# Optimization experiments

Hardware: AMD Instinct MI355X
Metric: run time of the kernel (lower is better)

The kernel has to match this reference:

```python
import jax, jax.numpy as jnp
import numpy as np

N = 50000      # nodes
E = 800000     # edges (before self loops)
F_IN = 128     # num_features
D = 128        # d_graph_layer
L = 3          # n_graph_layer (extra GAT layers after conv1)
DFC = 128      # d_FC_layer
NFC = 2        # n_FC_layer
C = 2          # num_classes
G = 1000       # number of graphs
NEG_SLOPE = 0.2


def setup_inputs() -> dict:
    key = jax.random.key(0)
    ks = jax.random.split(key, 24)
    s = lambda d: 1.0 / np.sqrt(d)
    inp = {
        "x": jax.random.normal(ks[0], (N, F_IN), jnp.float32),
        "energy": jax.random.normal(ks[1], (G, 1), jnp.float32),
        # conv1 params
        "W1": jax.random.normal(ks[2], (F_IN, D), jnp.float32) * s(F_IN),
        "as1": jax.random.normal(ks[3], (D,), jnp.float32) * s(D),
        "ad1": jax.random.normal(ks[4], (D,), jnp.float32) * s(D),
        "b1": jnp.zeros((D,), jnp.float32),
        # stacked convs params
        "Ws": jax.random.normal(ks[5], (L, D, D), jnp.float32) * s(D),
        "ass": jax.random.normal(ks[6], (L, D), jnp.float32) * s(D),
        "ads": jax.random.normal(ks[7], (L, D), jnp.float32) * s(D),
        "bs": jnp.zeros((L, D), jnp.float32),
        # FC head
        "lin0_W": jax.random.normal(ks[8], (D, DFC), jnp.float32) * s(D),
        "lin0_b": jnp.zeros((DFC,), jnp.float32),
        "lin1_W": jax.random.normal(ks[9], (DFC + 1, DFC), jnp.float32) * s(DFC + 1),
        "lin1_b": jnp.zeros((DFC,), jnp.float32),
        "lins_W": jax.random.normal(ks[10], (NFC - 1, DFC, DFC), jnp.float32) * s(DFC),
        "lins_b": jnp.zeros((NFC - 1, DFC), jnp.float32),
        "lin3_W": jax.random.normal(ks[11], (DFC, C), jnp.float32) * s(DFC),
        "lin3_b": jnp.zeros((C,), jnp.float32),
        # graph structure
        "edge_index": jax.random.randint(ks[12], (2, E), 0, N, dtype=jnp.int64),
        "batchs": jnp.sort(jax.random.randint(ks[13], (N,), 0, G, dtype=jnp.int64)),
    }
    return inp


def gat_layer(x, W, a_src, a_dst, b, src, dst):
    # GATConv (heads=1): h = xW; e_ij = LeakyReLU(a_src.h_src + a_dst.h_dst);
    # alpha = softmax over edges grouped by dst; out_i = sum alpha * h_src + b
    h = x @ W                                        # [N, D]
    e = jax.nn.leaky_relu((h @ a_src)[src] + (h @ a_dst)[dst], NEG_SLOPE)  # [E']
    m = jax.ops.segment_max(e, dst, num_segments=N)  # every node has a self loop
    w = jnp.exp(e - m[dst])
    denom = jax.ops.segment_sum(w, dst, num_segments=N)
    alpha = w / denom[dst]
    out = jax.ops.segment_sum(h[src] * alpha[:, None], dst, num_segments=N)
    return out + b


def reference(x, energy, W1, as1, ad1, b1, Ws, ass, ads, bs,
              lin0_W, lin0_b, lin1_W, lin1_b, lins_W, lins_b,
              lin3_W, lin3_b, edge_index, batchs):
    loop = jnp.arange(N, dtype=edge_index.dtype)     # GATConv add_self_loops
    src = jnp.concatenate([edge_index[0], loop])
    dst = jnp.concatenate([edge_index[1], loop])

    h = jax.nn.relu(gat_layer(x, W1, as1, ad1, b1, src, dst))
    for i in range(L):
        h = jax.nn.relu(gat_layer(h, Ws[i], ass[i], ads[i], bs[i], src, dst))

    g = jax.ops.segment_sum(h, batchs, num_segments=G)   # global_add_pool [G, D]
    y = jax.nn.relu(g @ lin0_W + lin0_b)                 # lins[0]
    z = jax.nn.relu(jnp.concatenate([y, energy], axis=1) @ lin1_W + lin1_b)
    z = z + y                                            # residual
    for i in range(NFC - 1):
        z = jax.nn.relu(z @ lins_W[i] + lins_b[i])
    logits = z @ lin3_W + lin3_b
    return jax.nn.log_softmax(logits, axis=1)            # last == 'log'
```

## Files before the change

kernel.cpp:

```cpp
#include <hip/hip_runtime.h>
#include <math.h>

#define NN 50000
#define EE 800000
#define ET 850000
#define DD 128
#define GG 1000
#define SLOPE 0.2f

#define KB   2048
#define NBA  416
#define BSZ  4096
#define NBUK 208

#define LSTR 136

typedef unsigned int  u32;
typedef unsigned short u16;
typedef _Float16 f16;
typedef __attribute__((ext_vector_type(8))) _Float16 f16x8;
typedef __attribute__((ext_vector_type(4))) float f32x4;

__device__ __forceinline__ u16 f2h(float f){
  return __builtin_bit_cast(unsigned short, (_Float16)f);
}
__device__ __forceinline__ float hlo(u32 d){
  return (float)__builtin_bit_cast(_Float16, (unsigned short)(d & 0xFFFFu));
}
__device__ __forceinline__ float hhi(u32 d){
  return (float)__builtin_bit_cast(_Float16, (unsigned short)(d >> 16));
}

__global__ void init_k(const int* __restrict__ batchs, int* __restrict__ cnt,
                       int* __restrict__ gstart, int* __restrict__ bcur){
  int n = blockIdx.x*256 + threadIdx.x;
  if (n < NBUK) bcur[n] = 0;
  if (n < NN){
    cnt[n] = 0;
    int b = batchs[n];
    int prev = n ? batchs[n-1] : -1;
    for (int g = prev+1; g <= b; ++g) gstart[g] = n;
    if (n == NN-1){
      for (int g = b+1; g <= GG; ++g) gstart[g] = NN;
    }
  }
}

__global__ void count_k(const int* __restrict__ ei, int* __restrict__ cnt,
                        int* __restrict__ rank){
  int e = blockIdx.x*256 + threadIdx.x;
  if (e < ET){
    int d = (e < EE) ? ei[EE + e] : (e - EE);
    rank[e] = atomicAdd(&cnt[d], 1);
  }
}

__global__ __launch_bounds__(256) void blocksum_k(const int* __restrict__ cnt,
                                                  int* __restrict__ bsum){
  int i = blockIdx.x*256 + threadIdx.x;
  int v = (i < NN) ? cnt[i] : 0;
  #pragma unroll
  for (int o=32;o;o>>=1) v += __shfl_xor(v,o);
  __shared__ int ws[4];
  if ((threadIdx.x & 63) == 0) ws[threadIdx.x>>6] = v;
  __syncthreads();
  if (threadIdx.x == 0) bsum[blockIdx.x] = ws[0]+ws[1]+ws[2]+ws[3];
}

__global__ __launch_bounds__(256) void scanb_k(int* __restrict__ bsum, int nb){
  int tid = threadIdx.x;
  int v = (tid < nb) ? bsum[tid] : 0;
  int lane = tid & 63, wv = tid >> 6;
  int s = v;
  #pragma unroll
  for (int o=1;o<64;o<<=1){ int t = __shfl_up(s,o); if (lane>=o) s += t; }
  __shared__ int ws[4];
  if (lane == 63) ws[wv] = s;
  __syncthreads();
  int woff = 0;
  for (int k=0;k<wv;++k) woff += ws[k];
  if (tid < nb) bsum[tid] = s - v + woff;
}

__global__ __launch_bounds__(256) void scatter_k(const int* __restrict__ cnt,
                                                 const int* __restrict__ bsum,
                                                 int* __restrict__ row_start){
  int i = blockIdx.x*256 + threadIdx.x;
  int v = (i < NN) ? cnt[i] : 0;
  int lane = threadIdx.x & 63, wv = threadIdx.x >> 6;
  int s = v;
  #pragma unroll
  for (int o=1;o<64;o<<=1){ int t = __shfl_up(s,o); if (lane>=o) s += t; }
  __shared__ int ws[4];
  if (lane == 63) ws[wv] = s;
  __syncthreads();
  int woff = 0;
  for (int k=0;k<wv;++k) woff += ws[k];
  int off = s - v + woff + bsum[blockIdx.x];
  if (i < NN) row_start[i] = off;
  if (i == 0) row_start[NN] = ET;
}

__global__ __launch_bounds__(256) void partA_k(const int* __restrict__ ei,
                                               const int* __restrict__ rank,
                                               const int* __restrict__ row_start,
                                               int* __restrict__ bcur,
                                               uint2* __restrict__ stage){
  __shared__ uint2 lpairs[KB];
  __shared__ int lcnt[256], lstart[256], lrun[256], gbase[256];
  __shared__ int ws[4];
  int tid = threadIdx.x;
  int base = blockIdx.x * KB;
  int nE = min(KB, ET - base);
  lcnt[tid] = 0;
  __syncthreads();
  u32 pos_r[KB/256]; u32 src_r[KB/256];
  #pragma unroll
  for (int i=0;i<KB/256;++i){
    int e = base + i*256 + tid;
    u32 p = 0xFFFFFFFFu, s = 0;
    if (e < ET){
      int d, sr;
      if (e < EE){ sr = ei[e]; d = ei[EE + e]; }
      else       { sr = e - EE; d = sr; }
      p = (u32)(row_start[d] + rank[e]);
      s = (u32)sr;
      atomicAdd(&lcnt[p >> 12], 1);
    }
    pos_r[i] = p; src_r[i] = s;
  }
  __syncthreads();
  int v = lcnt[tid];
  int lane = tid & 63, wv = tid >> 6;
  int s = v;
  #pragma unroll
  for (int o=1;o<64;o<<=1){ int t = __shfl_up(s,o); if (lane>=o) s += t; }
  if (lane == 63) ws[wv] = s;
  __syncthreads();
  int woff = 0;
  for (int k=0;k<wv;++k) woff += ws[k];
  int excl = s - v + woff;
  lstart[tid] = excl;
  lrun[tid]   = excl;
  gbase[tid]  = (tid < NBUK && v > 0) ? atomicAdd(&bcur[tid], v) : 0;
  __syncthreads();
  #pragma unroll
  for (int i=0;i<KB/256;++i){
    if (pos_r[i] != 0xFFFFFFFFu){
      int b = pos_r[i] >> 12;
      int slot = atomicAdd(&lrun[b], 1);
      lpairs[slot] = make_uint2(pos_r[i], src_r[i]);
    }
  }
  __syncthreads();
  for (int j = tid; j < nE; j += 256){
    uint2 pr = lpairs[j];
    int b = pr.x >> 12;
    int dest = (b << 12) + gbase[b] + (j - lstart[b]);
    stage[dest] = pr;
  }
}

__global__ __launch_bounds__(256) void partB_k(const uint2* __restrict__ stage,
                                               int* __restrict__ srcs){
  __shared__ int buf[BSZ];
  int b = blockIdx.x, tid = threadIdx.x;
  int base = b << 12;
  int n_b = min(BSZ, ET - base);
  for (int j = tid; j < n_b; j += 256){
    uint2 pr = stage[base + j];
    buf[pr.x - base] = (int)pr.y;
  }
  __syncthreads();
  for (int j = tid; j*4 < n_b; j += 256){
    *(int4*)(srcs + base + j*4) = *(const int4*)(buf + j*4);
  }
}

__global__ __launch_bounds__(256) void gemm_mfma_k(const float* __restrict__ A,
                                                   const float* __restrict__ W,
                                                   const float* __restrict__ as,
                                                   const float* __restrict__ ad,
                                                   u16* __restrict__ Ch,
                                                   float* __restrict__ hs,
                                                   float* __restrict__ hd){
  __shared__ u16 Al[64*LSTR];
  __shared__ u16 Wt[128*LSTR];
  int tid = threadIdx.x;
  int rbase = blockIdx.x*64;

  #pragma unroll
  for (int it=0; it<8; ++it){
    int i = it*256 + tid;
    int r = i >> 5, c4 = i & 31;
    float4 v = {0.f,0.f,0.f,0.f};
    if (rbase + r < NN) v = *(const float4*)(A + (size_t)(rbase+r)*DD + c4*4);
    u32 p0 = (u32)f2h(v.x) | ((u32)f2h(v.y) << 16);
    u32 p1 = (u32)f2h(v.z) | ((u32)f2h(v.w) << 16);
    *(u32*)(&Al[r*LSTR + c4*4])     = p0;
    *(u32*)(&Al[r*LSTR + c4*4 + 2]) = p1;
  }
  #pragma unroll
  for (int it=0; it<16; ++it){
    int i = it*256 + tid;
    int k = i >> 5, c4 = i & 31;
    float4 v = *(const float4*)(W + (size_t)k*DD + c4*4);
    Wt[(c4*4+0)*LSTR + k] = f2h(v.x);
    Wt[(c4*4+1)*LSTR + k] = f2h(v.y);
    Wt[(c4*4+2)*LSTR + k] = f2h(v.z);
    Wt[(c4*4+3)*LSTR + k] = f2h(v.w);
  }
  __syncthreads();

  int wid = tid >> 6;
  int l   = tid & 63;
  int lr  = l & 15;
  int lk  = l >> 4;

  f32x4 acc[8] = {};
  #pragma unroll
  for (int ks=0; ks<4; ++ks){
    int k0 = ks*32;
    f16x8 a = *(const f16x8*)(&Al[(wid*16+lr)*LSTR + k0 + lk*8]);
    #pragma unroll
    for (int ct=0; ct<8; ++ct){
      f16x8 b = *(const f16x8*)(&Wt[(ct*16+lr)*LSTR + k0 + lk*8]);
      acc[ct] = __builtin_amdgcn_mfma_f32_16x16x32_f16(a, b, acc[ct], 0, 0, 0);
    }
  }

  float hsum[4] = {0.f,0.f,0.f,0.f};
  float hdsum[4] = {0.f,0.f,0.f,0.f};
  #pragma unroll
  for (int ct=0; ct<8; ++ct){
    float a_s = as[ct*16 + lr];
    float a_d = ad[ct*16 + lr];
    #pragma unroll
    for (int i=0;i<4;++i){
      hsum[i]  += acc[ct][i]*a_s;
      hdsum[i] += acc[ct][i]*a_d;
    }
  }
  #pragma unroll
  for (int i=0;i<4;++i){
    #pragma unroll
    for (int o=1;o<16;o<<=1){
      hsum[i]  += __shfl_xor(hsum[i],  o);
      hdsum[i] += __shfl_xor(hdsum[i], o);
    }
  }
  if (lr == 0){
    #pragma unroll
    for (int i=0;i<4;++i){
      int r = rbase + wid*16 + lk*4 + i;
      if (r < NN){ hs[r] = hsum[i]; hd[r] = hdsum[i]; }
    }
  }
  #pragma unroll
  for (int i=0;i<4;++i){
    int r = rbase + wid*16 + lk*4 + i;
    if (r < NN){
      #pragma unroll
      for (int ct=0; ct<8; ++ct)
        Ch[(size_t)r*DD + ct*16 + lr] = f2h(acc[ct][i]);
    }
  }
}

__global__ __launch_bounds__(256) void gat_agg_h_k(const u16* __restrict__ hh,
                                                   const float* __restrict__ hs,
                                                   const float* __restrict__ hd,
                                                   const int* __restrict__ row_start,
                                                   const int* __restrict__ srcs,
                                                   const float* __restrict__ bias,
                                                   float* __restrict__ out){
  int node = blockIdx.x*4 + (threadIdx.x >> 6);
  int lane = threadIdx.x & 63;
  if (node >= NN) return;
  int half = lane >> 5;
  int hl   = lane & 31;
  int beg = row_start[node], end = row_start[node+1];
  float hdn = hd[node];
  float m = -INFINITY, denom = 0.f;
  float a0=0.f, a1=0.f, a2=0.f, a3=0.f;
  for (int c=beg; c<end; c+=64){
    int nc = min(64, end-c);
    float e = -INFINITY; int src = 0;
    if (lane < nc){
      src = srcs[c+lane];
      float t = hs[src] + hdn;
      e = (t >= 0.f) ? t : SLOPE*t;
    }
    float cm = e;
    #pragma unroll
    for (int o=32;o;o>>=1) cm = fmaxf(cm, __shfl_xor(cm,o));
    float nm = fmaxf(m, cm);
    float w = (lane < nc) ? expf(e - nm) : 0.f;
    float cs = w;
    #pragma unroll
    for (int o=32;o;o>>=1) cs += __shfl_xor(cs,o);
    float scale = expf(m - nm);
    denom = denom*scale + cs;
    a0 *= scale; a1 *= scale; a2 *= scale; a3 *= scale;
    m = nm;
    int nh = (nc + 1 - half) >> 1;
    for (int i=0;i<nh;++i){
      int j = 2*i + half;
      float wi = __shfl(w, j);
      int   si = __shfl(src, j);
      uint2 hv = *(const uint2*)(hh + (size_t)si*DD + hl*4);
      a0 += wi*hlo(hv.x); a1 += wi*hhi(hv.x);
      a2 += wi*hlo(hv.y); a3 += wi*hhi(hv.y);
    }
  }
  a0 += __shfl_xor(a0, 32);
  a1 += __shfl_xor(a1, 32);
  a2 += __shfl_xor(a2, 32);
  a3 += __shfl_xor(a3, 32);
  if (half == 0){
    float inv = 1.f/denom;
    float4 b4 = *(const float4*)(bias + hl*4);
    float4 o4;
    o4.x = fmaxf(a0*inv + b4.x, 0.f);
    o4.y = fmaxf(a1*inv + b4.y, 0.f);
    o4.z = fmaxf(a2*inv + b4.z, 0.f);
    o4.w = fmaxf(a3*inv + b4.w, 0.f);
    *(float4*)(out + (size_t)node*DD + hl*4) = o4;
  }
}

__global__ __launch_bounds__(128) void tail_k(const float* __restrict__ h,
                                              const int* __restrict__ gstart,
                                              const float* __restrict__ energy,
                                              const float* __restrict__ W0, const float* __restrict__ b0,
                                              const float* __restrict__ W1, const float* __restrict__ b1,
                                              const float* __restrict__ W2, const float* __restrict__ b2,
                                              const float* __restrict__ W3, const float* __restrict__ b3,
                                              float* __restrict__ out){
  __shared__ float row[DD];
  __shared__ float buf[DD];
  int gr = blockIdx.x, j = threadIdx.x;
  int beg = gstart[gr], end = gstart[gr+1];
  float s = 0.f;
  for (int n=beg; n<end; ++n) s += h[(size_t)n*DD + j];
  row[j] = s;
  __syncthreads();
  float acc = 0.f;
  #pragma unroll 8
  for (int k=0;k<DD;++k) acc += row[k]*W0[k*DD + j];
  float y = fmaxf(acc + b0[j], 0.f);
  buf[j] = y;
  __syncthreads();
  acc = 0.f;
  #pragma unroll 8
  for (int k=0;k<DD;++k) acc += buf[k]*W1[k*DD + j];
  acc += energy[gr]*W1[DD*DD + j];
  float z = fmaxf(acc + b1[j], 0.f) + y;
  __syncthreads();
  row[j] = z;
  __syncthreads();
  acc = 0.f;
  #pragma unroll 8
  for (int k=0;k<DD;++k) acc += row[k]*W2[k*DD + j];
  float z2 = fmaxf(acc + b2[j], 0.f);
  buf[j] = z2;
  __syncthreads();
  if (j < 64){
    float za = buf[j], zb = buf[j+64];
    float l0 = za*W3[j*2]     + zb*W3[(j+64)*2];
    float l1 = za*W3[j*2 + 1] + zb*W3[(j+64)*2 + 1];
    #pragma unroll
    for (int o=32;o;o>>=1){ l0 += __shfl_xor(l0,o); l1 += __shfl_xor(l1,o); }
    if (j == 0){
      l0 += b3[0]; l1 += b3[1];
      float mx = fmaxf(l0, l1);
      float lse = mx + logf(expf(l0-mx) + expf(l1-mx));
      out[gr*2]   = l0 - lse;
      out[gr*2+1] = l1 - lse;
    }
  }
}

extern "C" void kernel_launch(void* const* d_in, const int* in_sizes, int n_in,
                              void* d_out, int out_size, void* d_ws, size_t ws_size,
                              hipStream_t stream) {
  const float* x      = (const float*)d_in[0];
  const float* energy = (const float*)d_in[1];
  const float* W1     = (const float*)d_in[2];
  const float* as1    = (const float*)d_in[3];
  const float* ad1    = (const float*)d_in[4];
  const float* b1     = (const float*)d_in[5];
  const float* Ws     = (const float*)d_in[6];
  const float* ass    = (const float*)d_in[7];
  const float* ads    = (const float*)d_in[8];
  const float* bs     = (const float*)d_in[9];
  const float* lin0_W = (const float*)d_in[10];
  const float* lin0_b = (const float*)d_in[11];
  const float* lin1_W = (const float*)d_in[12];
  const float* lin1_b = (const float*)d_in[13];
  const float* lins_W = (const float*)d_in[14];
  const float* lins_b = (const float*)d_in[15];
  const float* lin3_W = (const float*)d_in[16];
  const float* lin3_b = (const float*)d_in[17];
  const int*   ei     = (const int*)d_in[18];
  const int*   batchs = (const int*)d_in[19];
  float* out = (float*)d_out;

  char* wp = (char*)d_ws;
  auto alloc = [&](size_t bytes)->void*{
    void* p = (void*)wp;
    wp += (bytes + 255) & ~(size_t)255;
    return p;
  };
  float* hA        = (float*)alloc((size_t)NN*DD*4);
  float* hB        = (float*)alloc((size_t)NN*DD*4);
  u16*   hHf       = (u16*)hB;
  float* hs        = (float*)alloc((size_t)NN*4);
  float* hd        = (float*)alloc((size_t)NN*4);
  int*   cnt       = (int*)alloc((size_t)NN*4);
  int*   row_start = (int*)alloc((size_t)(NN+1)*4);
  int*   rank      = (int*)alloc((size_t)ET*4);
  int*   srcs      = (int*)alloc((size_t)ET*4);
  uint2* stage     = (uint2*)alloc((size_t)NBUK*BSZ*8);
  int*   bcur      = (int*)alloc((size_t)NBUK*4);
  int*   gstart    = (int*)alloc((size_t)(GG+1)*4);
  int*   bsum      = (int*)alloc((size_t)256*4);

  const int NB_N  = (NN + 255)/256;
  const int NB_E  = (ET + 255)/256;
  const int NB_W  = (NN + 3)/4;
  const int NB_G  = (NN + 63)/64;

  init_k<<<NB_N, 256, 0, stream>>>(batchs, cnt, gstart, bcur);
  count_k<<<NB_E, 256, 0, stream>>>(ei, cnt, rank);
  blocksum_k<<<NB_N, 256, 0, stream>>>(cnt, bsum);
  scanb_k<<<1, 256, 0, stream>>>(bsum, NB_N);
  scatter_k<<<NB_N, 256, 0, stream>>>(cnt, bsum, row_start);
  partA_k<<<NBA, 256, 0, stream>>>(ei, rank, row_start, bcur, stage);
  partB_k<<<NBUK, 256, 0, stream>>>(stage, srcs);

  gemm_mfma_k<<<NB_G, 256, 0, stream>>>(x, W1, as1, ad1, hHf, hs, hd);
  gat_agg_h_k<<<NB_W, 256, 0, stream>>>(hHf, hs, hd, row_start, srcs, b1, hA);
  for (int l=1; l<4; ++l){
    const float* Wl  = Ws  + (size_t)(l-1)*DD*DD;
    const float* asl = ass + (size_t)(l-1)*DD;
    const float* adl = ads + (size_t)(l-1)*DD;
    const float* bl  = bs  + (size_t)(l-1)*DD;
    gemm_mfma_k<<<NB_G, 256, 0, stream>>>(hA, Wl, asl, adl, hHf, hs, hd);
    gat_agg_h_k<<<NB_W, 256, 0, stream>>>(hHf, hs, hd, row_start, srcs, bl, hA);
  }

  tail_k<<<GG, 128, 0, stream>>>(hA, gstart, energy,
                                 lin0_W, lin0_b, lin1_W, lin1_b,
                                 lins_W, lins_b, lin3_W, lin3_b, out);
}
```

Measured before the change: 481.8 us.

## Store activations in fp16 and pre-transpose weights; GEMM reads operands directly

```diff
diff --git a/kernel.cpp b/kernel.cpp
--- a/kernel.cpp
+++ b/kernel.cpp
@@ -13,8 +13,6 @@
 #define BSZ  4096
 #define NBUK 208
 
-#define LSTR 136
-
 typedef unsigned int  u32;
 typedef unsigned short u16;
 typedef _Float16 f16;
@@ -29,6 +27,9 @@
 }
 __device__ __forceinline__ float hhi(u32 d){
   return (float)__builtin_bit_cast(_Float16, (unsigned short)(d >> 16));
+}
+__device__ __forceinline__ float h2f(u16 h){
+  return (float)__builtin_bit_cast(_Float16, h);
 }
 
 __global__ void init_k(const int* __restrict__ batchs, int* __restrict__ cnt,
@@ -177,55 +178,58 @@
   }
 }
 
-__global__ __launch_bounds__(256) void gemm_mfma_k(const float* __restrict__ A,
-                                                   const float* __restrict__ W,
-                                                   const float* __restrict__ as,
-                                                   const float* __restrict__ ad,
-                                                   u16* __restrict__ Ch,
-                                                   float* __restrict__ hs,
-                                                   float* __restrict__ hd){
-  __shared__ u16 Al[64*LSTR];
-  __shared__ u16 Wt[128*LSTR];
+__global__ __launch_bounds__(256) void wcvt_k(const float* __restrict__ W1,
+                                              const float* __restrict__ Ws,
+                                              u16* __restrict__ Wt4){
+  int g = blockIdx.x*256 + threadIdx.x;
+  int l = g >> 14;
+  int rem = g & 16383;
+  int n = rem >> 7, k = rem & 127;
+  float v = (l == 0) ? W1[k*DD + n] : Ws[(size_t)(l-1)*DD*DD + k*DD + n];
+  Wt4[(size_t)l*DD*DD + n*DD + k] = f2h(v);
+}
+
+__global__ __launch_bounds__(256) void xcvt_k(const float* __restrict__ x,
+                                              u16* __restrict__ xh){
+  int i = blockIdx.x*256 + threadIdx.x;
+  if (i*4 < NN*DD){
+    float4 v = *(const float4*)(x + (size_t)i*4);
+    u32 p0 = (u32)f2h(v.x) | ((u32)f2h(v.y) << 16);
+    u32 p1 = (u32)f2h(v.z) | ((u32)f2h(v.w) << 16);
+    *(u32*)(xh + (size_t)i*4)     = p0;
+    *(u32*)(xh + (size_t)i*4 + 2) = p1;
+  }
+}
+
+__global__ __launch_bounds__(256) void gemm_direct_k(const u16* __restrict__ Ah,
+                                                     const u16* __restrict__ Wt,
+                                                     const float* __restrict__ as,
+                                                     const float* __restrict__ ad,
+                                                     u16* __restrict__ Ch,
+                                                     float* __restrict__ hs,
+                                                     float* __restrict__ hd){
   int tid = threadIdx.x;
   int rbase = blockIdx.x*64;
-
-  #pragma unroll
-  for (int it=0; it<8; ++it){
-    int i = it*256 + tid;
-    int r = i >> 5, c4 = i & 31;
-    float4 v = {0.f,0.f,0.f,0.f};
-    if (rbase + r < NN) v = *(const float4*)(A + (size_t)(rbase+r)*DD + c4*4);
-    u32 p0 = (u32)f2h(v.x) | ((u32)f2h(v.y) << 16);
-    u32 p1 = (u32)f2h(v.z) | ((u32)f2h(v.w) << 16);
-    *(u32*)(&Al[r*LSTR + c4*4])     = p0;
-    *(u32*)(&Al[r*LSTR + c4*4 + 2]) = p1;
-  }
-  #pragma unroll
-  for (int it=0; it<16; ++it){
-    int i = it*256 + tid;
-    int k = i >> 5, c4 = i & 31;
-    float4 v = *(const float4*)(W + (size_t)k*DD + c4*4);
-    Wt[(c4*4+0)*LSTR + k] = f2h(v.x);
-    Wt[(c4*4+1)*LSTR + k] = f2h(v.y);
-    Wt[(c4*4+2)*LSTR + k] = f2h(v.z);
-    Wt[(c4*4+3)*LSTR + k] = f2h(v.w);
-  }
-  __syncthreads();
-
   int wid = tid >> 6;
   int l   = tid & 63;
   int lr  = l & 15;
   int lk  = l >> 4;
+  int arow = rbase + wid*16 + lr;
+
+  f16x8 a[4] = {};
+  if (arow < NN){
+    #pragma unroll
+    for (int ks=0; ks<4; ++ks)
+      a[ks] = *(const f16x8*)(Ah + (size_t)arow*DD + ks*32 + lk*8);
+  }
 
   f32x4 acc[8] = {};
   #pragma unroll
-  for (int ks=0; ks<4; ++ks){
-    int k0 = ks*32;
-    f16x8 a = *(const f16x8*)(&Al[(wid*16+lr)*LSTR + k0 + lk*8]);
-    #pragma unroll
-    for (int ct=0; ct<8; ++ct){
-      f16x8 b = *(const f16x8*)(&Wt[(ct*16+lr)*LSTR + k0 + lk*8]);
-      acc[ct] = __builtin_amdgcn_mfma_f32_16x16x32_f16(a, b, acc[ct], 0, 0, 0);
+  for (int ct=0; ct<8; ++ct){
+    #pragma unroll
+    for (int ks=0; ks<4; ++ks){
+      f16x8 b = *(const f16x8*)(Wt + (size_t)(ct*16+lr)*DD + ks*32 + lk*8);
+      acc[ct] = __builtin_amdgcn_mfma_f32_16x16x32_f16(a[ks], b, acc[ct], 0, 0, 0);
     }
   }
 
@@ -273,7 +277,7 @@
                                                    const int* __restrict__ row_start,
                                                    const int* __restrict__ srcs,
                                                    const float* __restrict__ bias,
-                                                   float* __restrict__ out){
+                                                   u16* __restrict__ out){
   int node = blockIdx.x*4 + (threadIdx.x >> 6);
   int lane = threadIdx.x & 63;
   if (node >= NN) return;
@@ -320,16 +324,16 @@
   if (half == 0){
     float inv = 1.f/denom;
     float4 b4 = *(const float4*)(bias + hl*4);
-    float4 o4;
-    o4.x = fmaxf(a0*inv + b4.x, 0.f);
-    o4.y = fmaxf(a1*inv + b4.y, 0.f);
-    o4.z = fmaxf(a2*inv + b4.z, 0.f);
-    o4.w = fmaxf(a3*inv + b4.w, 0.f);
-    *(float4*)(out + (size_t)node*DD + hl*4) = o4;
-  }
-}
-
-__global__ __launch_bounds__(128) void tail_k(const float* __restrict__ h,
+    ushort4 o4;
+    o4.x = f2h(fmaxf(a0*inv + b4.x, 0.f));
+    o4.y = f2h(fmaxf(a1*inv + b4.y, 0.f));
+    o4.z = f2h(fmaxf(a2*inv + b4.z, 0.f));
+    o4.w = f2h(fmaxf(a3*inv + b4.w, 0.f));
+    *(ushort4*)(out + (size_t)node*DD + hl*4) = o4;
+  }
+}
+
+__global__ __launch_bounds__(128) void tail_k(const u16* __restrict__ h,
                                               const int* __restrict__ gstart,
                                               const float* __restrict__ energy,
                                               const float* __restrict__ W0, const float* __restrict__ b0,
@@ -342,7 +346,7 @@
   int gr = blockIdx.x, j = threadIdx.x;
   int beg = gstart[gr], end = gstart[gr+1];
   float s = 0.f;
-  for (int n=beg; n<end; ++n) s += h[(size_t)n*DD + j];
+  for (int n=beg; n<end; ++n) s += h2f(h[(size_t)n*DD + j]);
   row[j] = s;
   __syncthreads();
   float acc = 0.f;
@@ -412,9 +416,10 @@
     wp += (bytes + 255) & ~(size_t)255;
     return p;
   };
-  float* hA        = (float*)alloc((size_t)NN*DD*4);
-  float* hB        = (float*)alloc((size_t)NN*DD*4);
-  u16*   hHf       = (u16*)hB;
+  u16*   hA16      = (u16*)alloc((size_t)NN*DD*2);
+  u16*   hB16      = (u16*)alloc((size_t)NN*DD*2);
+  u16*   xh        = (u16*)alloc((size_t)NN*DD*2);
+  u16*   Wt4       = (u16*)alloc((size_t)4*DD*DD*2);
   float* hs        = (float*)alloc((size_t)NN*4);
   float* hd        = (float*)alloc((size_t)NN*4);
   int*   cnt       = (int*)alloc((size_t)NN*4);
@@ -430,6 +435,7 @@
   const int NB_E  = (ET + 255)/256;
   const int NB_W  = (NN + 3)/4;
   const int NB_G  = (NN + 63)/64;
+  const int NB_X  = (NN*DD/4 + 255)/256;
 
   init_k<<<NB_N, 256, 0, stream>>>(batchs, cnt, gstart, bcur);
   count_k<<<NB_E, 256, 0, stream>>>(ei, cnt, rank);
@@ -438,19 +444,21 @@
   scatter_k<<<NB_N, 256, 0, stream>>>(cnt, bsum, row_start);
   partA_k<<<NBA, 256, 0, stream>>>(ei, rank, row_start, bcur, stage);
   partB_k<<<NBUK, 256, 0, stream>>>(stage, srcs);
-
-  gemm_mfma_k<<<NB_G, 256, 0, stream>>>(x, W1, as1, ad1, hHf, hs, hd);
-  gat_agg_h_k<<<NB_W, 256, 0, stream>>>(hHf, hs, hd, row_start, srcs, b1, hA);
+  wcvt_k<<<(4*DD*DD)/256, 256, 0, stream>>>(W1, Ws, Wt4);
+  xcvt_k<<<NB_X, 256, 0, stream>>>(x, xh);
+
+  gemm_direct_k<<<NB_G, 256, 0, stream>>>(xh, Wt4, as1, ad1, hB16, hs, hd);
+  gat_agg_h_k<<<NB_W, 256, 0, stream>>>(hB16, hs, hd, row_start, srcs, b1, hA16);
   for (int l=1; l<4; ++l){
-    const float* Wl  = Ws  + (size_t)(l-1)*DD*DD;
+    const u16*   Wtl = Wt4 + (size_t)l*DD*DD;
     const float* asl = ass + (size_t)(l-1)*DD;
     const float* adl = ads + (size_t)(l-1)*DD;
     const float* bl  = bs  + (size_t)(l-1)*DD;
-    gemm_mfma_k<<<NB_G, 256, 0, stream>>>(hA, Wl, asl, adl, hHf, hs, hd);
-    gat_agg_h_k<<<NB_W, 256, 0, stream>>>(hHf, hs, hd, row_start, srcs, bl, hA);
-  }
-
-  tail_k<<<GG, 128, 0, stream>>>(hA, gstart, energy,
+    gemm_direct_k<<<NB_G, 256, 0, stream>>>(hA16, Wtl, asl, adl, hB16, hs, hd);
+    gat_agg_h_k<<<NB_W, 256, 0, stream>>>(hB16, hs, hd, row_start, srcs, bl, hA16);
+  }
+
+  tail_k<<<GG, 128, 0, stream>>>(hA16, gstart, energy,
                                  lin0_W, lin0_b, lin1_W, lin1_b,
                                  lins_W, lins_b, lin3_W, lin3_b, out);
 }
```

Result: no change. 486.4 us (+1.0%).
